# Optimization experiments

Hardware: AMD Instinct MI355X
Metric: run time of the kernel (lower is better)

## Reference

```python
import jax, jax.numpy as jnp
import numpy as np

B, S, D, H = 2, 2048, 1024, 16
DH = D // H


def setup_inputs() -> dict:
    key = jax.random.key(0)
    ks = jax.random.split(key, 5)
    scale = 1.0 / np.sqrt(D)
    return {
        "x": jax.random.normal(ks[0], (B, S, D), dtype=jnp.float32),
        "Wq": jax.random.normal(ks[1], (D, D), dtype=jnp.float32) * scale,
        "bq": jnp.zeros((D,), jnp.float32),
        "Wk": jax.random.normal(ks[2], (D, D), dtype=jnp.float32) * scale,
        "bk": jnp.zeros((D,), jnp.float32),
        "Wv": jax.random.normal(ks[3], (D, D), dtype=jnp.float32) * scale,
        "bv": jnp.zeros((D,), jnp.float32),
        "Wo": jax.random.normal(ks[4], (D, D), dtype=jnp.float32) * scale,
        "bo": jnp.zeros((D,), jnp.float32),
    }


def reference(x, Wq, bq, Wk, bk, Wv, bv, Wo, bo):
    b, s, d = x.shape
    # QKV projections (torch Linear: x @ W.T + b)
    q = (x @ Wq.T + bq).reshape(b, s, H, DH).transpose(0, 2, 1, 3)  # [b,h,s,dh]
    k = (x @ Wk.T + bk).reshape(b, s, H, DH).transpose(0, 2, 1, 3)
    v = (x @ Wv.T + bv).reshape(b, s, H, DH).transpose(0, 2, 1, 3)
    scale = 1.0 / jnp.sqrt(jnp.array(DH, dtype=jnp.float32))
    energy = jnp.einsum("bhqd,bhkd->bhqk", q, k) * scale  # [b,h,s,s]
    attn = jax.nn.softmax(energy, axis=-1)
    out = jnp.einsum("bhqk,bhkd->bhqd", attn, v)  # [b,h,s,dh]
    out = out.transpose(0, 2, 1, 3).reshape(b, s, d)
    return out @ Wo.T + bo
```

## Files before the change

### kernel.cpp

```cpp
#include <hip/hip_runtime.h>

using bf16x8 = __attribute__((ext_vector_type(8))) short;
using f32x4  = __attribute__((ext_vector_type(4))) float;
using u32x2  = __attribute__((ext_vector_type(2))) unsigned int;

__device__ __forceinline__ unsigned short f2bf(float f) {
  union { float f; unsigned int u; } v; v.f = f;
  unsigned int u = v.u;
  unsigned int r = (u + 0x7FFFu + ((u >> 16) & 1u)) >> 16;
  return (unsigned short)r;
}

__device__ __forceinline__ unsigned int pk2bf(float a, float b) {
  union { float f; unsigned int u; } x, y; x.f = a; y.f = b;
  unsigned int ua = x.u + 0x7FFFu + ((x.u >> 16) & 1u);
  unsigned int ub = y.u + 0x7FFFu + ((y.u >> 16) & 1u);
  return __builtin_amdgcn_perm(ub, ua, 0x07060302u);
}

__device__ __forceinline__ void gl_lds16(const void* g, void* l) {
  __builtin_amdgcn_global_load_lds(
      (const __attribute__((address_space(1))) void*)g,
      (__attribute__((address_space(3))) void*)l, 16, 0, 0);
}

__global__ void cast_all(const float* __restrict__ x,
                         const float* __restrict__ wq, const float* __restrict__ wk,
                         const float* __restrict__ wv, const float* __restrict__ wo,
                         unsigned short* __restrict__ xb,
                         unsigned short* __restrict__ wqb, unsigned short* __restrict__ wkb,
                         unsigned short* __restrict__ wvb, unsigned short* __restrict__ wob) {
  size_t i4 = ((size_t)blockIdx.x * 256 + threadIdx.x) * 4;
  const float* src; unsigned short* dst; size_t off;
  if (i4 < 4194304) { src = x; dst = xb; off = i4; }
  else {
    size_t j = i4 - 4194304;
    int w = (int)(j >> 20);
    off = j & 1048575;
    src = (w == 0) ? wq : (w == 1) ? wk : (w == 2) ? wv : wo;
    dst = (w == 0) ? wqb : (w == 1) ? wkb : (w == 2) ? wvb : wob;
  }
  float4 v = *(const float4*)(src + off);
  ushort4 o;
  o.x = f2bf(v.x); o.y = f2bf(v.y); o.z = f2bf(v.z); o.w = f2bf(v.w);
  *(ushort4*)(dst + off) = o;
}

template <int BN>
__device__ __forceinline__ void gemm_tile_nt(const unsigned short* __restrict__ A,
                                             const unsigned short* __restrict__ Bm,
                                             int tile_m, int tile_n,
                                             f32x4 acc[4][BN / 32]) {
  constexpr int JN = BN / 32;
  __shared__ __align__(16) unsigned short As[128 * 32];
  __shared__ __align__(16) unsigned short Bs[BN * 32];
  const int tid = threadIdx.x;
  const int lane = tid & 63, wave = tid >> 6;
  const int quad = lane >> 4, l16 = lane & 15;
  const int wm = (wave & 1) * 64, wn = (wave >> 1) * (BN / 2);
  const int srow = tid >> 2;
  const int scol = (tid & 3) * 8;

#pragma unroll
  for (int i = 0; i < 4; i++)
#pragma unroll
    for (int j = 0; j < JN; j++)
#pragma unroll
      for (int r = 0; r < 4; r++) acc[i][j][r] = 0.f;

  for (int k0 = 0; k0 < 1024; k0 += 32) {
#pragma unroll
    for (int t = 0; t < 2; t++)
      gl_lds16(A + (size_t)(tile_m + t * 64 + srow) * 1024 + k0 + scol,
               (char*)As + t * 4096 + tid * 16);
    if (BN == 128) {
#pragma unroll
      for (int t = 0; t < 2; t++)
        gl_lds16(Bm + (size_t)(tile_n + t * 64 + srow) * 1024 + k0 + scol,
                 (char*)Bs + t * 4096 + tid * 16);
    } else {
      gl_lds16(Bm + (size_t)(tile_n + srow) * 1024 + k0 + scol, (char*)Bs + tid * 16);
    }
    __syncthreads();
    bf16x8 a[4], b[JN];
#pragma unroll
    for (int i = 0; i < 4; i++)
      a[i] = *(const bf16x8*)((const char*)As + ((wm + i * 16 + l16) * 32 + quad * 8) * 2);
#pragma unroll
    for (int j = 0; j < JN; j++)
      b[j] = *(const bf16x8*)((const char*)Bs + ((wn + j * 16 + l16) * 32 + quad * 8) * 2);
#pragma unroll
    for (int i = 0; i < 4; i++)
#pragma unroll
      for (int j = 0; j < JN; j++)
        acc[i][j] = __builtin_amdgcn_mfma_f32_16x16x32_bf16(a[i], b[j], acc[i][j], 0, 0, 0);
    __syncthreads();
  }
}

__global__ __launch_bounds__(256) void gemm_qkv(
    const unsigned short* __restrict__ xb,
    const unsigned short* __restrict__ wqb, const unsigned short* __restrict__ wkb,
    const unsigned short* __restrict__ wvb,
    const float* __restrict__ bq, const float* __restrict__ bk, const float* __restrict__ bv,
    unsigned short* __restrict__ Qo, unsigned short* __restrict__ Ko,
    unsigned short* __restrict__ Vt) {
  const int z = blockIdx.z;
  const unsigned short* Bm = (z == 0) ? wqb : (z == 1) ? wkb : wvb;
  const float* bias = (z == 0) ? bq : (z == 1) ? bk : bv;
  const int tile_m = blockIdx.y * 128, tile_n = blockIdx.x * 128;
  f32x4 acc[4][4];
  gemm_tile_nt<128>(xb, Bm, tile_m, tile_n, acc);

  const int tid = threadIdx.x, lane = tid & 63, wave = tid >> 6;
  const int quad = lane >> 4, l16 = lane & 15;
  const int wm = (wave & 1) * 64, wn = (wave >> 1) * 64;
  const float scale = (z == 0) ? 0.125f : 1.0f;

  if (z < 2) {
    unsigned short* out = (z == 0) ? Qo : Ko;
#pragma unroll
    for (int i = 0; i < 4; i++)
#pragma unroll
      for (int j = 0; j < 4; j++) {
        int n = tile_n + wn + j * 16 + l16;
        float bn = bias[n];
#pragma unroll
        for (int r = 0; r < 4; r++) {
          int m = tile_m + wm + i * 16 + quad * 4 + r;
          out[(size_t)m * 1024 + n] = f2bf((acc[i][j][r] + bn) * scale);
        }
      }
  } else {
#pragma unroll
    for (int i = 0; i < 4; i++)
#pragma unroll
      for (int j = 0; j < 4; j++) {
        int n = tile_n + wn + j * 16 + l16;
        int hh = n >> 6, dh = n & 63;
        float bn = bias[n];
        int m0 = tile_m + wm + i * 16 + quad * 4;
        int b = m0 >> 11, s = m0 & 2047;
        ushort4 pk;
        pk.x = f2bf(acc[i][j][0] + bn);
        pk.y = f2bf(acc[i][j][1] + bn);
        pk.z = f2bf(acc[i][j][2] + bn);
        pk.w = f2bf(acc[i][j][3] + bn);
        *(ushort4*)(Vt + ((size_t)((b * 16 + hh) * 64 + dh)) * 2048 + s) = pk;
      }
  }
}

__global__ __launch_bounds__(256, 2) void flash_attn(
    const unsigned short* __restrict__ Qg, const unsigned short* __restrict__ Kg,
    const unsigned short* __restrict__ Vt, unsigned short* __restrict__ AO) {
  __shared__ __align__(16) unsigned short KV[2][16384];
  __shared__ __align__(16) unsigned short Pc[4][32][40];

  const int tid = threadIdx.x, lane = tid & 63, wave = tid >> 6;
  const int quad = lane >> 4, l16 = lane & 15;
  const int bi = blockIdx.x;
  const int bh = (bi & 7) * 4 + ((bi >> 3) & 3);
  const int qt = bi >> 5;
  const int b = bh >> 4, h = bh & 15;

  const size_t qbase = ((size_t)(b * 2048 + qt * 128 + wave * 32)) * 1024 + h * 64;
  bf16x8 qf[2][2];
#pragma unroll
  for (int qs = 0; qs < 2; qs++)
#pragma unroll
    for (int ks = 0; ks < 2; ks++)
      qf[qs][ks] = *(const bf16x8*)(Qg + qbase + (size_t)(qs * 16 + l16) * 1024 +
                                    ks * 32 + quad * 8);

  f32x4 O[2][4];
  float lp[2] = {0.f, 0.f};
#pragma unroll
  for (int qs = 0; qs < 2; qs++)
#pragma unroll
    for (int mb = 0; mb < 4; mb++)
#pragma unroll
      for (int r = 0; r < 4; r++) O[qs][mb][r] = 0.f;

  const size_t kbase = (size_t)(b * 2048) * 1024 + h * 64;
  const size_t vbase = (size_t)(bh * 64) * 2048;

  auto stage = [&](int kt) {
    char* Kl = (char*)&KV[kt & 1][0];
    char* Vl = (char*)&KV[kt & 1][8192];
#pragma unroll
    for (int t = 0; t < 4; t++) {
      int i = t * 256 + tid; int g = i >> 7, row = i & 127;
      gl_lds16(Kg + kbase + (size_t)(kt * 128 + row) * 1024 + g * 8, Kl + i * 16);
    }
#pragma unroll
    for (int t = 0; t < 4; t++) {
      int i = t * 256 + tid; int g = i >> 6, d = i & 63;
      gl_lds16(Vt + vbase + (size_t)d * 2048 + kt * 128 + g * 8, Vl + i * 16);
    }
  };

  stage(0);

  for (int kt = 0; kt < 16; kt++) {
    __syncthreads();
    if (kt < 15) stage(kt + 1);
    __builtin_amdgcn_sched_barrier(0);

    const char* Kl = (const char*)&KV[kt & 1][0];
    const char* Vl = (const char*)&KV[kt & 1][8192];

    f32x4 sacc[2][8];
#pragma unroll
    for (int qs = 0; qs < 2; qs++)
#pragma unroll
      for (int nb = 0; nb < 8; nb++)
#pragma unroll
        for (int r = 0; r < 4; r++) sacc[qs][nb][r] = 0.f;
#pragma unroll
    for (int nb = 0; nb < 8; nb++) {
      bf16x8 kf0 = *(const bf16x8*)(Kl + ((quad) * 128 + nb * 16 + l16) * 16);
      bf16x8 kf1 = *(const bf16x8*)(Kl + ((4 + quad) * 128 + nb * 16 + l16) * 16);
#pragma unroll
      for (int qs = 0; qs < 2; qs++) {
        sacc[qs][nb] = __builtin_amdgcn_mfma_f32_16x16x32_bf16(kf0, qf[qs][0], sacc[qs][nb], 0, 0, 0);
        sacc[qs][nb] = __builtin_amdgcn_mfma_f32_16x16x32_bf16(kf1, qf[qs][1], sacc[qs][nb], 0, 0, 0);
      }
    }

    unsigned int pk[2][8][2];
#pragma unroll
    for (int qs = 0; qs < 2; qs++)
#pragma unroll
      for (int nb = 0; nb < 8; nb++) {
        float p0 = __expf(sacc[qs][nb][0]);
        float p1 = __expf(sacc[qs][nb][1]);
        float p2 = __expf(sacc[qs][nb][2]);
        float p3 = __expf(sacc[qs][nb][3]);
        lp[qs] += (p0 + p1) + (p2 + p3);
        pk[qs][nb][0] = pk2bf(p0, p1);
        pk[qs][nb][1] = pk2bf(p2, p3);
      }

#pragma unroll
    for (int kc = 0; kc < 4; kc++) {
#pragma unroll
      for (int qs = 0; qs < 2; qs++)
#pragma unroll
        for (int t = 0; t < 2; t++) {
          u32x2 d; d[0] = pk[qs][2 * kc + t][0]; d[1] = pk[qs][2 * kc + t][1];
          *(u32x2*)(&Pc[wave][qs * 16 + l16][t * 16 + quad * 4]) = d;
        }
      bf16x8 pf[2];
#pragma unroll
      for (int qs = 0; qs < 2; qs++)
        pf[qs] = *(const bf16x8*)(&Pc[wave][qs * 16 + l16][quad * 8]);
#pragma unroll
      for (int mb = 0; mb < 4; mb++) {
        bf16x8 vf = *(const bf16x8*)(Vl + ((kc * 4 + quad) * 64 + mb * 16 + l16) * 16);
#pragma unroll
        for (int qs = 0; qs < 2; qs++)
          O[qs][mb] = __builtin_amdgcn_mfma_f32_16x16x32_bf16(vf, pf[qs], O[qs][mb], 0, 0, 0);
      }
    }
  }

  float inv[2];
#pragma unroll
  for (int qs = 0; qs < 2; qs++) {
    float l = lp[qs];
    l += __shfl_xor(l, 16);
    l += __shfl_xor(l, 32);
    inv[qs] = 1.f / l;
  }

  unsigned short* Pw = (unsigned short*)&KV[0][0] + wave * (32 * 72);
#pragma unroll
  for (int qs = 0; qs < 2; qs++)
#pragma unroll
    for (int mb = 0; mb < 4; mb++) {
      u32x2 d;
      d[0] = pk2bf(O[qs][mb][0] * inv[qs], O[qs][mb][1] * inv[qs]);
      d[1] = pk2bf(O[qs][mb][2] * inv[qs], O[qs][mb][3] * inv[qs]);
      *(u32x2*)(Pw + (qs * 16 + l16) * 72 + mb * 16 + quad * 4) = d;
    }
  const size_t orow0 = (size_t)(b * 2048 + qt * 128 + wave * 32);
#pragma unroll
  for (int p = 0; p < 4; p++) {
    int q = p * 8 + (lane >> 3), dh = (lane & 7) * 8;
    bf16x8 o = *(const bf16x8*)(Pw + q * 72 + dh);
    *(bf16x8*)(AO + (orow0 + q) * 1024 + h * 64 + dh) = o;
  }
}

__global__ __launch_bounds__(256) void gemm_out(
    const unsigned short* __restrict__ AO, const unsigned short* __restrict__ wob,
    const float* __restrict__ bo, float* __restrict__ out) {
  const int tile_m = blockIdx.y * 128, tile_n = blockIdx.x * 64;
  f32x4 acc[4][2];
  gemm_tile_nt<64>(AO, wob, tile_m, tile_n, acc);
  const int tid = threadIdx.x, lane = tid & 63, wave = tid >> 6;
  const int quad = lane >> 4, l16 = lane & 15;
  const int wm = (wave & 1) * 64, wn = (wave >> 1) * 32;
#pragma unroll
  for (int i = 0; i < 4; i++)
#pragma unroll
    for (int j = 0; j < 2; j++) {
      int n = tile_n + wn + j * 16 + l16;
      float bn = bo[n];
#pragma unroll
      for (int r = 0; r < 4; r++) {
        int m = tile_m + wm + i * 16 + quad * 4 + r;
        out[(size_t)m * 1024 + n] = acc[i][j][r] + bn;
      }
    }
}

extern "C" void kernel_launch(void* const* d_in, const int* in_sizes, int n_in,
                              void* d_out, int out_size, void* d_ws, size_t ws_size,
                              hipStream_t stream) {
  (void)in_sizes; (void)n_in; (void)out_size; (void)ws_size;
  const float* x  = (const float*)d_in[0];
  const float* Wq = (const float*)d_in[1];
  const float* bq = (const float*)d_in[2];
  const float* Wk = (const float*)d_in[3];
  const float* bk = (const float*)d_in[4];
  const float* Wv = (const float*)d_in[5];
  const float* bv = (const float*)d_in[6];
  const float* Wo = (const float*)d_in[7];
  const float* bo = (const float*)d_in[8];
  float* out = (float*)d_out;

  char* ws = (char*)d_ws;
  unsigned short* xb  = (unsigned short*)(ws + 0);
  unsigned short* wqb = (unsigned short*)(ws + 8388608);
  unsigned short* wkb = (unsigned short*)(ws + 10485760);
  unsigned short* wvb = (unsigned short*)(ws + 12582912);
  unsigned short* wob = (unsigned short*)(ws + 14680064);
  unsigned short* Qb  = (unsigned short*)(ws + 16777216);
  unsigned short* Kb  = (unsigned short*)(ws + 25165824);
  unsigned short* Vtb = (unsigned short*)(ws + 33554432);
  unsigned short* AOb = (unsigned short*)(ws + 41943040);

  cast_all<<<8192, 256, 0, stream>>>(x, Wq, Wk, Wv, Wo, xb, wqb, wkb, wvb, wob);
  gemm_qkv<<<dim3(8, 32, 3), dim3(256), 0, stream>>>(xb, wqb, wkb, wvb, bq, bk, bv, Qb, Kb, Vtb);
  flash_attn<<<512, 256, 0, stream>>>(Qb, Kb, Vtb, AOb);
  gemm_out<<<dim3(16, 32, 1), dim3(256), 0, stream>>>(AOb, wob, bo, out);
}
```

Before: 219.7 us.

## Split flash attention block into 8 waves of 16 query rows each

The attention kernel now runs 512 threads per block (8 waves), with each wave handling 16 query rows instead of 32. Per-wave register use for Q fragments, score accumulators and output accumulators is halved, and launch bounds ask for 4 blocks per CU to raise occupancy and hide latency. The trade-off is that each K/V fragment read from LDS now feeds only one MFMA instead of two, which doubles LDS read traffic per FLOP. The staging loop is also re-split across the larger thread count.

```diff
diff --git a/kernel.cpp b/kernel.cpp
--- a/kernel.cpp
+++ b/kernel.cpp
@@ -151,11 +151,11 @@
   }
 }
 
-__global__ __launch_bounds__(256, 2) void flash_attn(
+__global__ __launch_bounds__(512, 4) void flash_attn(
     const unsigned short* __restrict__ Qg, const unsigned short* __restrict__ Kg,
     const unsigned short* __restrict__ Vt, unsigned short* __restrict__ AO) {
   __shared__ __align__(16) unsigned short KV[2][16384];
-  __shared__ __align__(16) unsigned short Pc[4][32][40];
+  __shared__ __align__(16) unsigned short Pc[8][16][40];
 
   const int tid = threadIdx.x, lane = tid & 63, wave = tid >> 6;
   const int quad = lane >> 4, l16 = lane & 15;
@@ -164,23 +164,18 @@
   const int qt = bi >> 5;
   const int b = bh >> 4, h = bh & 15;
 
-  const size_t qbase = ((size_t)(b * 2048 + qt * 128 + wave * 32)) * 1024 + h * 64;
-  bf16x8 qf[2][2];
-#pragma unroll
-  for (int qs = 0; qs < 2; qs++)
-#pragma unroll
-    for (int ks = 0; ks < 2; ks++)
-      qf[qs][ks] = *(const bf16x8*)(Qg + qbase + (size_t)(qs * 16 + l16) * 1024 +
-                                    ks * 32 + quad * 8);
-
-  f32x4 O[2][4];
-  float lp[2] = {0.f, 0.f};
-#pragma unroll
-  for (int qs = 0; qs < 2; qs++)
-#pragma unroll
-    for (int mb = 0; mb < 4; mb++)
-#pragma unroll
-      for (int r = 0; r < 4; r++) O[qs][mb][r] = 0.f;
+  const size_t qbase = ((size_t)(b * 2048 + qt * 128 + wave * 16)) * 1024 + h * 64;
+  bf16x8 qf[2];
+#pragma unroll
+  for (int ks = 0; ks < 2; ks++)
+    qf[ks] = *(const bf16x8*)(Qg + qbase + (size_t)l16 * 1024 + ks * 32 + quad * 8);
+
+  f32x4 O[4];
+  float lp = 0.f;
+#pragma unroll
+  for (int mb = 0; mb < 4; mb++)
+#pragma unroll
+    for (int r = 0; r < 4; r++) O[mb][r] = 0.f;
 
   const size_t kbase = (size_t)(b * 2048) * 1024 + h * 64;
   const size_t vbase = (size_t)(bh * 64) * 2048;
@@ -189,13 +184,13 @@
     char* Kl = (char*)&KV[kt & 1][0];
     char* Vl = (char*)&KV[kt & 1][8192];
 #pragma unroll
-    for (int t = 0; t < 4; t++) {
-      int i = t * 256 + tid; int g = i >> 7, row = i & 127;
+    for (int t = 0; t < 2; t++) {
+      int i = t * 512 + tid; int g = i >> 7, row = i & 127;
       gl_lds16(Kg + kbase + (size_t)(kt * 128 + row) * 1024 + g * 8, Kl + i * 16);
     }
 #pragma unroll
-    for (int t = 0; t < 4; t++) {
-      int i = t * 256 + tid; int g = i >> 6, d = i & 63;
+    for (int t = 0; t < 2; t++) {
+      int i = t * 512 + tid; int g = i >> 6, d = i & 63;
       gl_lds16(Vt + vbase + (size_t)d * 2048 + kt * 128 + g * 8, Vl + i * 16);
     }
   };
@@ -210,83 +205,63 @@
     const char* Kl = (const char*)&KV[kt & 1][0];
     const char* Vl = (const char*)&KV[kt & 1][8192];
 
-    f32x4 sacc[2][8];
-#pragma unroll
-    for (int qs = 0; qs < 2; qs++)
-#pragma unroll
-      for (int nb = 0; nb < 8; nb++)
-#pragma unroll
-        for (int r = 0; r < 4; r++) sacc[qs][nb][r] = 0.f;
+    f32x4 sacc[8];
+#pragma unroll
+    for (int nb = 0; nb < 8; nb++)
+#pragma unroll
+      for (int r = 0; r < 4; r++) sacc[nb][r] = 0.f;
 #pragma unroll
     for (int nb = 0; nb < 8; nb++) {
       bf16x8 kf0 = *(const bf16x8*)(Kl + ((quad) * 128 + nb * 16 + l16) * 16);
       bf16x8 kf1 = *(const bf16x8*)(Kl + ((4 + quad) * 128 + nb * 16 + l16) * 16);
-#pragma unroll
-      for (int qs = 0; qs < 2; qs++) {
-        sacc[qs][nb] = __builtin_amdgcn_mfma_f32_16x16x32_bf16(kf0, qf[qs][0], sacc[qs][nb], 0, 0, 0);
-        sacc[qs][nb] = __builtin_amdgcn_mfma_f32_16x16x32_bf16(kf1, qf[qs][1], sacc[qs][nb], 0, 0, 0);
-      }
-    }
-
-    unsigned int pk[2][8][2];
-#pragma unroll
-    for (int qs = 0; qs < 2; qs++)
-#pragma unroll
-      for (int nb = 0; nb < 8; nb++) {
-        float p0 = __expf(sacc[qs][nb][0]);
-        float p1 = __expf(sacc[qs][nb][1]);
-        float p2 = __expf(sacc[qs][nb][2]);
-        float p3 = __expf(sacc[qs][nb][3]);
-        lp[qs] += (p0 + p1) + (p2 + p3);
-        pk[qs][nb][0] = pk2bf(p0, p1);
-        pk[qs][nb][1] = pk2bf(p2, p3);
-      }
+      sacc[nb] = __builtin_amdgcn_mfma_f32_16x16x32_bf16(kf0, qf[0], sacc[nb], 0, 0, 0);
+      sacc[nb] = __builtin_amdgcn_mfma_f32_16x16x32_bf16(kf1, qf[1], sacc[nb], 0, 0, 0);
+    }
+
+    unsigned int pk[8][2];
+#pragma unroll
+    for (int nb = 0; nb < 8; nb++) {
+      float p0 = __expf(sacc[nb][0]);
+      float p1 = __expf(sacc[nb][1]);
+      float p2 = __expf(sacc[nb][2]);
+      float p3 = __expf(sacc[nb][3]);
+      lp += (p0 + p1) + (p2 + p3);
+      pk[nb][0] = pk2bf(p0, p1);
+      pk[nb][1] = pk2bf(p2, p3);
+    }
 
 #pragma unroll
     for (int kc = 0; kc < 4; kc++) {
 #pragma unroll
-      for (int qs = 0; qs < 2; qs++)
-#pragma unroll
-        for (int t = 0; t < 2; t++) {
-          u32x2 d; d[0] = pk[qs][2 * kc + t][0]; d[1] = pk[qs][2 * kc + t][1];
-          *(u32x2*)(&Pc[wave][qs * 16 + l16][t * 16 + quad * 4]) = d;
-        }
-      bf16x8 pf[2];
-#pragma unroll
-      for (int qs = 0; qs < 2; qs++)
-        pf[qs] = *(const bf16x8*)(&Pc[wave][qs * 16 + l16][quad * 8]);
+      for (int t = 0; t < 2; t++) {
+        u32x2 d; d[0] = pk[2 * kc + t][0]; d[1] = pk[2 * kc + t][1];
+        *(u32x2*)(&Pc[wave][l16][t * 16 + quad * 4]) = d;
+      }
+      bf16x8 pf = *(const bf16x8*)(&Pc[wave][l16][quad * 8]);
 #pragma unroll
       for (int mb = 0; mb < 4; mb++) {
         bf16x8 vf = *(const bf16x8*)(Vl + ((kc * 4 + quad) * 64 + mb * 16 + l16) * 16);
-#pragma unroll
-        for (int qs = 0; qs < 2; qs++)
-          O[qs][mb] = __builtin_amdgcn_mfma_f32_16x16x32_bf16(vf, pf[qs], O[qs][mb], 0, 0, 0);
-      }
-    }
-  }
-
-  float inv[2];
-#pragma unroll
-  for (int qs = 0; qs < 2; qs++) {
-    float l = lp[qs];
-    l += __shfl_xor(l, 16);
-    l += __shfl_xor(l, 32);
-    inv[qs] = 1.f / l;
-  }
-
-  unsigned short* Pw = (unsigned short*)&KV[0][0] + wave * (32 * 72);
-#pragma unroll
-  for (int qs = 0; qs < 2; qs++)
-#pragma unroll
-    for (int mb = 0; mb < 4; mb++) {
-      u32x2 d;
-      d[0] = pk2bf(O[qs][mb][0] * inv[qs], O[qs][mb][1] * inv[qs]);
-      d[1] = pk2bf(O[qs][mb][2] * inv[qs], O[qs][mb][3] * inv[qs]);
-      *(u32x2*)(Pw + (qs * 16 + l16) * 72 + mb * 16 + quad * 4) = d;
-    }
-  const size_t orow0 = (size_t)(b * 2048 + qt * 128 + wave * 32);
-#pragma unroll
-  for (int p = 0; p < 4; p++) {
+        O[mb] = __builtin_amdgcn_mfma_f32_16x16x32_bf16(vf, pf, O[mb], 0, 0, 0);
+      }
+    }
+  }
+
+  float l = lp;
+  l += __shfl_xor(l, 16);
+  l += __shfl_xor(l, 32);
+  float inv = 1.f / l;
+
+  unsigned short* Pw = (unsigned short*)&KV[0][0] + wave * (16 * 72);
+#pragma unroll
+  for (int mb = 0; mb < 4; mb++) {
+    u32x2 d;
+    d[0] = pk2bf(O[mb][0] * inv, O[mb][1] * inv);
+    d[1] = pk2bf(O[mb][2] * inv, O[mb][3] * inv);
+    *(u32x2*)(Pw + l16 * 72 + mb * 16 + quad * 4) = d;
+  }
+  const size_t orow0 = (size_t)(b * 2048 + qt * 128 + wave * 16);
+#pragma unroll
+  for (int p = 0; p < 2; p++) {
     int q = p * 8 + (lane >> 3), dh = (lane & 7) * 8;
     bf16x8 o = *(const bf16x8*)(Pw + q * 72 + dh);
     *(bf16x8*)(AO + (orow0 + q) * 1024 + h * 64 + dh) = o;
@@ -344,6 +319,6 @@
 
   cast_all<<<8192, 256, 0, stream>>>(x, Wq, Wk, Wv, Wo, xb, wqb, wkb, wvb, wob);
   gemm_qkv<<<dim3(8, 32, 3), dim3(256), 0, stream>>>(xb, wqb, wkb, wvb, bq, bk, bv, Qb, Kb, Vtb);
-  flash_attn<<<512, 256, 0, stream>>>(Qb, Kb, Vtb, AOb);
+  flash_attn<<<512, 512, 0, stream>>>(Qb, Kb, Vtb, AOb);
   gemm_out<<<dim3(16, 32, 1), dim3(256), 0, stream>>>(AOb, wob, bo, out);
 }
```

Result: no change. 216.6 us (-1.4%).
